# Optimization experiments

Measured on AMD Instinct MI355X. Metric: run time of the kernel, lower is better.

The kernel has to match this reference:

```python
import jax, jax.numpy as jnp
import numpy as np

B, N, DIN, DOUT = 8, 2048, 512, 256
NUM_BUCKETS = 20


def setup_inputs() -> dict:
    key = jax.random.key(0)
    ks = jax.random.split(key, 12)
    s_in = 1.0 / np.sqrt(DIN)
    s_out = 1.0 / np.sqrt(DOUT)
    return {
        "x": jax.random.normal(ks[0], (B, N, DIN), dtype=jnp.float32),
        "price_rank": jax.random.randint(ks[1], (B, N), 0, N, dtype=jnp.int64),
        "Wq": jax.random.uniform(ks[2], (DOUT, DIN), jnp.float32, -s_in, s_in),
        "bq": jax.random.uniform(ks[3], (DOUT,), jnp.float32, -s_in, s_in),
        "Wk": jax.random.uniform(ks[4], (DOUT, DIN), jnp.float32, -s_in, s_in),
        "bk": jax.random.uniform(ks[5], (DOUT,), jnp.float32, -s_in, s_in),
        "Wv": jax.random.uniform(ks[6], (DOUT, DIN), jnp.float32, -s_in, s_in),
        "bv": jax.random.uniform(ks[7], (DOUT,), jnp.float32, -s_in, s_in),
        "Ws": jax.random.uniform(ks[8], (1, DOUT), jnp.float32, -s_out, s_out),
        "bs": jax.random.uniform(ks[9], (1,), jnp.float32, -s_out, s_out),
        "rank_emb": jax.random.normal(ks[10], (NUM_BUCKETS, 1), dtype=jnp.float32),
        "rank_w": jnp.ones((1,), dtype=jnp.float32),
    }


def reference(x, price_rank, Wq, bq, Wk, bk, Wv, bv, Ws, bs, rank_emb, rank_w):
    scale = jnp.sqrt(jnp.asarray(DOUT, dtype=x.dtype))
    q = jnp.einsum("bnd,od->bno", x, Wq) + bq  # [B,N,DOUT]
    k = jnp.einsum("bnd,od->bno", x, Wk) + bk
    v = jnp.einsum("bnd,od->bno", x, Wv) + bv
    scores = jnp.einsum("bno,bmo->bnm", q, k) / scale  # [B,N,N]
    # learned pairwise rank-distance bias gate
    rank_dist = jnp.abs(price_rank[:, :, None] - price_rank[:, None, :])
    buckets = jnp.clip(rank_dist // 5, 0, NUM_BUCKETS - 1)  # [B,N,N] int
    prior = rank_emb[buckets, 0]  # gather embedding, squeeze last dim
    gate = jax.nn.sigmoid(rank_w[0] * prior)
    scores = scores * gate
    attn = jax.nn.softmax(scores, axis=2)
    context = jnp.einsum("bnm,bmo->bno", attn, v)  # [B,N,DOUT]
    winner = jax.nn.sigmoid(jnp.einsum("bno,uo->bnu", context, Ws) + bs)[..., 0]
    return winner  # [B,N]
```

## Files before the change

kernel.cpp:

```cpp
#include <hip/hip_runtime.h>
#include <hip/hip_bf16.h>

#define B_    8
#define N_    2048
#define DIN_  512
#define DOUT_ 256
#define NBUCK 20

typedef __attribute__((ext_vector_type(8))) short  short8;
typedef __attribute__((ext_vector_type(4))) float  floatx4;

__device__ __forceinline__ unsigned short f2b(float f) {
    __hip_bfloat16 h = __float2bfloat16(f);
    unsigned short u;
    __builtin_memcpy(&u, &h, 2);
    return u;
}

__device__ __forceinline__ void load_lds16(const unsigned short* g, unsigned short* l) {
    __builtin_amdgcn_global_load_lds(
        (const __attribute__((address_space(1))) unsigned int*)g,
        (__attribute__((address_space(3))) unsigned int*)l, 16, 0, 0);
}

__device__ __forceinline__ float fexp2(float x) {
    float r;
    asm("v_exp_f32 %0, %1" : "=v"(r) : "v"(x));
    return r;
}

__global__ __launch_bounds__(256) void prep_kernel(
    const float* __restrict__ Wv, const float* __restrict__ Ws,
    const float* __restrict__ bv,
    float* __restrict__ wvs, float* __restrict__ bvs) {
    const int blk = blockIdx.x, tid = threadIdx.x;
    __shared__ float wsl[DOUT_];
    wsl[tid] = Ws[tid];
    __syncthreads();
    if (tid < 128) {
        int d = blk * 128 + tid;
        float s0 = 0.f, s1 = 0.f, s2 = 0.f, s3 = 0.f;
#pragma unroll 8
        for (int o = 0; o < DOUT_; o += 4) {
            s0 += Wv[(size_t)(o + 0) * DIN_ + d] * wsl[o + 0];
            s1 += Wv[(size_t)(o + 1) * DIN_ + d] * wsl[o + 1];
            s2 += Wv[(size_t)(o + 2) * DIN_ + d] * wsl[o + 2];
            s3 += Wv[(size_t)(o + 3) * DIN_ + d] * wsl[o + 3];
        }
        wvs[d] = (s0 + s1) + (s2 + s3);
    }
    if (blk == 0 && tid < 64) {
        float bb = wsl[tid] * bv[tid] + wsl[tid + 64] * bv[tid + 64] +
                   wsl[tid + 128] * bv[tid + 128] + wsl[tid + 192] * bv[tid + 192];
        for (int off = 1; off < 64; off <<= 1) bb += __shfl_xor(bb, off, 64);
        if (tid == 0) *bvs = bb;
    }
}

__global__ __launch_bounds__(256) void cvt_x_kernel(const float* __restrict__ x,
                                                    const float* __restrict__ wvs,
                                                    const float* __restrict__ bvs,
                                                    const float* __restrict__ wq,
                                                    const float* __restrict__ wk,
                                                    unsigned short* __restrict__ xb,
                                                    unsigned short* __restrict__ wdst,
                                                    float* __restrict__ vw) {
    int tid = threadIdx.x;
    if (blockIdx.x >= 4096) {
        int i = ((blockIdx.x - 4096) * 256 + tid) * 8;
        const float* src = (i < 131072) ? (wq + i) : (wk + (i - 131072));
        float4 a = *(const float4*)(src);
        float4 b = *(const float4*)(src + 4);
        uint4 r;
        r.x = f2b(a.x) | ((unsigned)f2b(a.y) << 16);
        r.y = f2b(a.z) | ((unsigned)f2b(a.w) << 16);
        r.z = f2b(b.x) | ((unsigned)f2b(b.y) << 16);
        r.w = f2b(b.z) | ((unsigned)f2b(b.w) << 16);
        *(uint4*)(wdst + i) = r;
        return;
    }
    int wave = tid >> 6, lane = tid & 63;
    int row = blockIdx.x * 4 + wave;
    size_t base = (size_t)row * DIN_ + lane * 8;
    float4 a = *(const float4*)(x + base);
    float4 b = *(const float4*)(x + base + 4);
    float4 wa = *(const float4*)(wvs + lane * 8);
    float4 wb = *(const float4*)(wvs + lane * 8 + 4);
    uint4 r;
    r.x = f2b(a.x) | ((unsigned)f2b(a.y) << 16);
    r.y = f2b(a.z) | ((unsigned)f2b(a.w) << 16);
    r.z = f2b(b.x) | ((unsigned)f2b(b.y) << 16);
    r.w = f2b(b.z) | ((unsigned)f2b(b.w) << 16);
    *(uint4*)(xb + base) = r;
    float d = a.x * wa.x + a.y * wa.y + a.z * wa.z + a.w * wa.w +
              b.x * wb.x + b.y * wb.y + b.z * wb.z + b.w * wb.w;
    for (int off = 1; off < 64; off <<= 1) d += __shfl_xor(d, off, 64);
    if (lane == 0) vw[row] = d + *bvs;
}

__global__ __launch_bounds__(256, 2) void qkv_kernel(
    const unsigned short* __restrict__ xb, const unsigned short* __restrict__ wb,
    const float* __restrict__ bq, const float* __restrict__ bk,
    unsigned short* __restrict__ qo, unsigned short* __restrict__ ko) {
    __shared__ unsigned short alds[2][128 * 64];
    __shared__ unsigned short blds[2][128 * 64];
    const int g = blockIdx.x;
    const int xcd = g & 7, t2 = g >> 3;
    const int colBlk = t2 & 3, rowGrp = t2 >> 2;
    const int rowBlk = rowGrp * 8 + xcd;
    const int tid = threadIdx.x;
    const int wave = tid >> 6, lane = tid & 63, quad = lane >> 4, l16 = lane & 15;
    const int wr = wave >> 1, wc = wave & 1;
    const int row0 = rowBlk * 128, col0 = colBlk * 128;
    const int sw3 = l16 & 7;

    floatx4 acc[4][4];
#pragma unroll
    for (int i = 0; i < 4; ++i)
#pragma unroll
        for (int j = 0; j < 4; ++j) acc[i][j] = (floatx4){0.f, 0.f, 0.f, 0.f};

    const int gseg = (lane & 7) ^ (lane >> 3);
    const unsigned short* ag = xb + (size_t)(row0 + wave * 8 + (lane >> 3)) * DIN_ + gseg * 8;
    const unsigned short* bg = wb + (size_t)(col0 + wave * 8 + (lane >> 3)) * DIN_ + gseg * 8;

#pragma unroll
    for (int i = 0; i < 4; ++i) {
        load_lds16(ag + (size_t)i * 32 * DIN_, &alds[0][wave * 512 + i * 2048]);
        load_lds16(bg + (size_t)i * 32 * DIN_, &blds[0][wave * 512 + i * 2048]);
    }
    __syncthreads();

#pragma unroll 1
    for (int t = 0; t < 8; ++t) {
        const unsigned short* al = (t & 1) ? alds[1] : alds[0];
        const unsigned short* bl = (t & 1) ? blds[1] : blds[0];
        unsigned short* aln = (t & 1) ? &alds[0][0] : &alds[1][0];
        unsigned short* bln = (t & 1) ? &blds[0][0] : &blds[1][0];
        if (t < 7) {
            size_t koff = (size_t)(t + 1) * 64;
#pragma unroll
            for (int i = 0; i < 4; ++i) {
                load_lds16(ag + (size_t)i * 32 * DIN_ + koff, aln + wave * 512 + i * 2048);
                load_lds16(bg + (size_t)i * 32 * DIN_ + koff, bln + wave * 512 + i * 2048);
            }
        }
#pragma unroll
        for (int h = 0; h < 2; ++h) {
            short8 af[4], bf[4];
#pragma unroll
            for (int f = 0; f < 4; ++f) {
                int ar = wr * 64 + f * 16 + l16;
                int br = wc * 64 + f * 16 + l16;
                int s  = (h * 4 + quad) ^ sw3;
                af[f] = *(const short8*)&al[(size_t)ar * 64 + s * 8];
                bf[f] = *(const short8*)&bl[(size_t)br * 64 + s * 8];
            }
#pragma unroll
            for (int i = 0; i < 4; ++i)
#pragma unroll
                for (int j = 0; j < 4; ++j)
                    acc[i][j] = __builtin_amdgcn_mfma_f32_16x16x32_bf16(af[i], bf[j], acc[i][j], 0, 0, 0);
        }
        __syncthreads();
    }

#pragma unroll
    for (int j = 0; j < 4; ++j) {
        int col = col0 + wc * 64 + j * 16 + l16;
        unsigned short* dst = (col < 256) ? qo : ko;
        float bias = (col < 256) ? bq[col] : bk[col - 256];
        int c = col & 255;
#pragma unroll
        for (int i = 0; i < 4; ++i)
#pragma unroll
            for (int r = 0; r < 4; ++r) {
                int row = row0 + wr * 64 + i * 16 + quad * 4 + r;
                dst[(size_t)row * DOUT_ + c] = f2b(acc[i][j][r] + bias);
            }
    }
}

__global__ __launch_bounds__(512, 2) void attn_kernel(
    const unsigned short* __restrict__ q, const unsigned short* __restrict__ k,
    const float* __restrict__ vw, const int* __restrict__ pr,
    const float* __restrict__ rank_emb, const float* __restrict__ rank_w,
    const float* __restrict__ bs, float* __restrict__ out) {
    const int g = blockIdx.x;
    const int b = g & 7, rblk = g >> 3;
    const int tid = threadIdx.x, wave = tid >> 6, lane = tid & 63;
    const int quad = lane >> 4, l16 = lane & 15;
    const int n0 = rblk * 64;
    const int rg = wave >> 2, ch = wave & 3;

    __shared__ unsigned short kbuf[2][32768];
    __shared__ float gtab_r[NBUCK * 32];
    __shared__ float lL[8][32], wdL[8][32];

    for (int t = tid; t < NBUCK * 32; t += 512)
        gtab_r[t] = 0.0625f * 1.44269504f /
                    (1.f + __expf(-rank_w[0] * rank_emb[t >> 5]));

    const unsigned short* qb = q + (size_t)b * N_ * DOUT_;
    const unsigned short* kb = k + (size_t)b * N_ * DOUT_;
    const float* vwb = vw + b * N_;
    const int* prb = pr + b * N_;
    const int l8 = lane & 7;
    const int l31 = lane & 31;

    short8 qf[2][8];
#pragma unroll
    for (int a = 0; a < 2; ++a)
#pragma unroll
        for (int c = 0; c < 8; ++c)
            qf[a][c] = *(const short8*)(qb + (size_t)(n0 + rg * 32 + a * 16 + l16) * DOUT_ + c * 32 + quad * 8);

    float prn5[2][4];
#pragma unroll
    for (int a = 0; a < 2; ++a)
#pragma unroll
        for (int r = 0; r < 4; ++r)
            prn5[a][r] = (float)prb[n0 + rg * 32 + a * 16 + quad * 4 + r] * 0.2f;

    float lacc[2][4], wacc[2][4];
#pragma unroll
    for (int a = 0; a < 2; ++a)
#pragma unroll
        for (int r = 0; r < 4; ++r) { lacc[a][r] = 0.f; wacc[a][r] = 0.f; }

    const int stg_rbase = wave * 2 + (lane >> 5);
    const int stg_gseg  = (lane & 31) ^ (stg_rbase & 7);
    const unsigned short* stg_src0 = kb + (size_t)stg_rbase * DOUT_ + stg_gseg * 8;
    unsigned short* sdst0 = &kbuf[0][wave * 512];
    unsigned short* sdst1 = &kbuf[1][wave * 512];

    auto stage = [&](int j, unsigned short* sdst) {
        const unsigned short* src = stg_src0 + (size_t)j * 128 * DOUT_;
#pragma unroll
        for (int i = 0; i < 8; ++i)
            load_lds16(src + (size_t)i * 4096, sdst + i * 4096);
    };
    auto mfma = [&](floatx4 (&s)[2][2], const unsigned short* buf) {
#pragma unroll
        for (int a = 0; a < 2; ++a)
#pragma unroll
            for (int cf = 0; cf < 2; ++cf) s[a][cf] = (floatx4){0.f, 0.f, 0.f, 0.f};
        __builtin_amdgcn_s_setprio(1);
#pragma unroll
        for (int c = 0; c < 8; ++c) {
            int seg = (c * 4 + quad) ^ l8;
            short8 kf0 = *(const short8*)&buf[(size_t)(ch * 32 + l16) * 256 + seg * 8];
            short8 kf1 = *(const short8*)&buf[(size_t)(ch * 32 + 16 + l16) * 256 + seg * 8];
            s[0][0] = __builtin_amdgcn_mfma_f32_16x16x32_bf16(qf[0][c], kf0, s[0][0], 0, 0, 0);
            s[1][0] = __builtin_amdgcn_mfma_f32_16x16x32_bf16(qf[1][c], kf0, s[1][0], 0, 0, 0);
            s[0][1] = __builtin_amdgcn_mfma_f32_16x16x32_bf16(qf[0][c], kf1, s[0][1], 0, 0, 0);
            s[1][1] = __builtin_amdgcn_mfma_f32_16x16x32_bf16(qf[1][c], kf1, s[1][1], 0, 0, 0);
        }
        __builtin_amdgcn_s_setprio(0);
    };
    auto gate = [&](floatx4 (&s)[2][2], int pm0, int pm1, float w0, float w1) {
        float pm5_0 = (float)pm0 * 0.2f, pm5_1 = (float)pm1 * 0.2f;
#pragma unroll
        for (int a = 0; a < 2; ++a)
#pragma unroll
            for (int r = 0; r < 4; ++r) {
                float d0 = fabsf(prn5[a][r] - pm5_0);
                int i0 = (int)fminf(d0, 19.0f);
                float p0 = fexp2(s[a][0][r] * gtab_r[i0 * 32 + l31]);
                lacc[a][r] += p0;
                wacc[a][r] += p0 * w0;
                float d1 = fabsf(prn5[a][r] - pm5_1);
                int i1 = (int)fminf(d1, 19.0f);
                float p1 = fexp2(s[a][1][r] * gtab_r[i1 * 32 + l31]);
                lacc[a][r] += p1;
                wacc[a][r] += p1 * w1;
            }
    };

    floatx4 sA[2][2], sB[2][2];
    const int colq = ch * 32 + l16;

    stage(0, sdst0);
    int   pmA0 = prb[colq], pmA1 = prb[colq + 16];
    float wA0 = vwb[colq], wA1 = vwb[colq + 16];
    __syncthreads();
    stage(1, sdst1);
    int   pmB0 = prb[128 + colq], pmB1 = prb[128 + colq + 16];
    float wB0 = vwb[128 + colq], wB1 = vwb[128 + colq + 16];
    mfma(sA, kbuf[0]);
    __syncthreads();

#pragma unroll 1
    for (int jj = 0; jj < 7; ++jj) {
        {
            int jn = 2 * jj + 2;
            stage(jn, sdst0);
            int   p0 = prb[jn * 128 + colq], p1 = prb[jn * 128 + colq + 16];
            float w0 = vwb[jn * 128 + colq], w1 = vwb[jn * 128 + colq + 16];
            mfma(sB, kbuf[1]);
            __builtin_amdgcn_sched_barrier(0);
            gate(sA, pmA0, pmA1, wA0, wA1);
            pmA0 = p0; pmA1 = p1; wA0 = w0; wA1 = w1;
            __syncthreads();
        }
        {
            int jn = 2 * jj + 3;
            stage(jn, sdst1);
            int   p0 = prb[jn * 128 + colq], p1 = prb[jn * 128 + colq + 16];
            float w0 = vwb[jn * 128 + colq], w1 = vwb[jn * 128 + colq + 16];
            mfma(sA, kbuf[0]);
            __builtin_amdgcn_sched_barrier(0);
            gate(sB, pmB0, pmB1, wB0, wB1);
            pmB0 = p0; pmB1 = p1; wB0 = w0; wB1 = w1;
            __syncthreads();
        }
    }
    mfma(sB, kbuf[1]);
    __builtin_amdgcn_sched_barrier(0);
    gate(sA, pmA0, pmA1, wA0, wA1);
    gate(sB, pmB0, pmB1, wB0, wB1);

#pragma unroll
    for (int off = 1; off < 16; off <<= 1) {
#pragma unroll
        for (int a = 0; a < 2; ++a)
#pragma unroll
            for (int r = 0; r < 4; ++r) {
                lacc[a][r] += __shfl_xor(lacc[a][r], off, 64);
                wacc[a][r] += __shfl_xor(wacc[a][r], off, 64);
            }
    }
    if (l16 == 0) {
#pragma unroll
        for (int a = 0; a < 2; ++a)
#pragma unroll
            for (int r = 0; r < 4; ++r) {
                int row = a * 16 + quad * 4 + r;
                lL[wave][row]  = lacc[a][r];
                wdL[wave][row] = wacc[a][r];
            }
    }
    __syncthreads();
    if (tid < 64) {
        int rg2 = tid >> 5, sub = tid & 31;
        float l = 0.f, wd = 0.f;
#pragma unroll
        for (int c2 = 0; c2 < 4; ++c2) {
            l  += lL[rg2 * 4 + c2][sub];
            wd += wdL[rg2 * 4 + c2][sub];
        }
        float logit = wd / l + bs[0];
        out[(size_t)b * N_ + n0 + tid] = 1.f / (1.f + __expf(-logit));
    }
}

extern "C" void kernel_launch(void* const* d_in, const int* in_sizes, int n_in,
                              void* d_out, int out_size, void* d_ws, size_t ws_size,
                              hipStream_t stream) {
    const float* x   = (const float*)d_in[0];
    const int*   pr  = (const int*)d_in[1];
    const float* Wq  = (const float*)d_in[2];
    const float* bq  = (const float*)d_in[3];
    const float* Wk  = (const float*)d_in[4];
    const float* bk  = (const float*)d_in[5];
    const float* Wv  = (const float*)d_in[6];
    const float* bv  = (const float*)d_in[7];
    const float* Ws  = (const float*)d_in[8];
    const float* bs  = (const float*)d_in[9];
    const float* remb = (const float*)d_in[10];
    const float* rw   = (const float*)d_in[11];
    float* out = (float*)d_out;

    char* ws = (char*)d_ws;
    unsigned short* xb  = (unsigned short*)ws;
    unsigned short* wb  = (unsigned short*)(ws + 16777216);
    unsigned short* q   = (unsigned short*)(ws + 17301504);
    unsigned short* kk  = (unsigned short*)(ws + 25690112);
    float*          vwp = (float*)(ws + 34078720);
    float*          wvs = (float*)(ws + 34144256);
    float*          bvs = (float*)(ws + 34146304);

    hipLaunchKernelGGL(prep_kernel, dim3(4), dim3(256), 0, stream,
                       Wv, Ws, bv, wvs, bvs);
    hipLaunchKernelGGL(cvt_x_kernel, dim3(4224), dim3(256), 0, stream,
                       x, wvs, bvs, Wq, Wk, xb, wb, vwp);
    hipLaunchKernelGGL(qkv_kernel, dim3(512), dim3(256), 0, stream,
                       xb, wb, bq, bk, q, kk);
    hipLaunchKernelGGL(attn_kernel, dim3(256), dim3(512), 0, stream,
                       q, kk, vwp, pr, remb, rw, bs, out);
}
```

Measured before the change: 146.0 us.

## Fuse fp32-to-bf16 conversion and v·Ws projection into QKV GEMM kernel

Removes the separate conversion kernel and converts x and Wq/Wk from fp32 to bf16 while staging them into LDS inside the QKV GEMM. The fused v-projection dot product is accumulated by the column-block-0 workgroups. This drops the bf16 x and weight round trip through global memory and one launch. In exchange, each x row is read as fp32 by four column blocks, conversion is done in registers through a register-staged pipeline instead of direct global-to-LDS loads, and register pressure rises.

```diff
diff --git a/kernel.cpp b/kernel.cpp
--- a/kernel.cpp
+++ b/kernel.cpp
@@ -57,53 +57,15 @@
     }
 }
 
-__global__ __launch_bounds__(256) void cvt_x_kernel(const float* __restrict__ x,
-                                                    const float* __restrict__ wvs,
-                                                    const float* __restrict__ bvs,
-                                                    const float* __restrict__ wq,
-                                                    const float* __restrict__ wk,
-                                                    unsigned short* __restrict__ xb,
-                                                    unsigned short* __restrict__ wdst,
-                                                    float* __restrict__ vw) {
-    int tid = threadIdx.x;
-    if (blockIdx.x >= 4096) {
-        int i = ((blockIdx.x - 4096) * 256 + tid) * 8;
-        const float* src = (i < 131072) ? (wq + i) : (wk + (i - 131072));
-        float4 a = *(const float4*)(src);
-        float4 b = *(const float4*)(src + 4);
-        uint4 r;
-        r.x = f2b(a.x) | ((unsigned)f2b(a.y) << 16);
-        r.y = f2b(a.z) | ((unsigned)f2b(a.w) << 16);
-        r.z = f2b(b.x) | ((unsigned)f2b(b.y) << 16);
-        r.w = f2b(b.z) | ((unsigned)f2b(b.w) << 16);
-        *(uint4*)(wdst + i) = r;
-        return;
-    }
-    int wave = tid >> 6, lane = tid & 63;
-    int row = blockIdx.x * 4 + wave;
-    size_t base = (size_t)row * DIN_ + lane * 8;
-    float4 a = *(const float4*)(x + base);
-    float4 b = *(const float4*)(x + base + 4);
-    float4 wa = *(const float4*)(wvs + lane * 8);
-    float4 wb = *(const float4*)(wvs + lane * 8 + 4);
-    uint4 r;
-    r.x = f2b(a.x) | ((unsigned)f2b(a.y) << 16);
-    r.y = f2b(a.z) | ((unsigned)f2b(a.w) << 16);
-    r.z = f2b(b.x) | ((unsigned)f2b(b.y) << 16);
-    r.w = f2b(b.z) | ((unsigned)f2b(b.w) << 16);
-    *(uint4*)(xb + base) = r;
-    float d = a.x * wa.x + a.y * wa.y + a.z * wa.z + a.w * wa.w +
-              b.x * wb.x + b.y * wb.y + b.z * wb.z + b.w * wb.w;
-    for (int off = 1; off < 64; off <<= 1) d += __shfl_xor(d, off, 64);
-    if (lane == 0) vw[row] = d + *bvs;
-}
-
-__global__ __launch_bounds__(256, 2) void qkv_kernel(
-    const unsigned short* __restrict__ xb, const unsigned short* __restrict__ wb,
-    const float* __restrict__ bq, const float* __restrict__ bk,
-    unsigned short* __restrict__ qo, unsigned short* __restrict__ ko) {
-    __shared__ unsigned short alds[2][128 * 64];
-    __shared__ unsigned short blds[2][128 * 64];
+__global__ __launch_bounds__(256, 2) void qkvx_kernel(
+    const float* __restrict__ x, const float* __restrict__ wq,
+    const float* __restrict__ wk, const float* __restrict__ bq,
+    const float* __restrict__ bk, const float* __restrict__ wvs,
+    const float* __restrict__ bvs, unsigned short* __restrict__ qo,
+    unsigned short* __restrict__ ko, float* __restrict__ vw) {
+    __shared__ unsigned short alds[2][8192];
+    __shared__ unsigned short blds[2][8192];
+    __shared__ float wsl[DIN_];
     const int g = blockIdx.x;
     const int xcd = g & 7, t2 = g >> 3;
     const int colBlk = t2 & 3, rowGrp = t2 >> 2;
@@ -114,21 +76,84 @@
     const int row0 = rowBlk * 128, col0 = colBlk * 128;
     const int sw3 = l16 & 7;
 
+    wsl[tid] = wvs[tid];
+    wsl[tid + 256] = wvs[tid + 256];
+
+    const int sr = tid >> 1, h2 = tid & 1, r7 = sr & 7;
+    const float* asrc = x + (size_t)(row0 + sr) * DIN_ + h2 * 32;
+    const float* bsrc = (colBlk < 2 ? wq + (size_t)(col0 + sr) * DIN_
+                                    : wk + (size_t)(col0 + sr - 256) * DIN_) + h2 * 32;
+
     floatx4 acc[4][4];
 #pragma unroll
     for (int i = 0; i < 4; ++i)
 #pragma unroll
         for (int j = 0; j < 4; ++j) acc[i][j] = (floatx4){0.f, 0.f, 0.f, 0.f};
 
-    const int gseg = (lane & 7) ^ (lane >> 3);
-    const unsigned short* ag = xb + (size_t)(row0 + wave * 8 + (lane >> 3)) * DIN_ + gseg * 8;
-    const unsigned short* bg = wb + (size_t)(col0 + wave * 8 + (lane >> 3)) * DIN_ + gseg * 8;
-
-#pragma unroll
-    for (int i = 0; i < 4; ++i) {
-        load_lds16(ag + (size_t)i * 32 * DIN_, &alds[0][wave * 512 + i * 2048]);
-        load_lds16(bg + (size_t)i * 32 * DIN_, &blds[0][wave * 512 + i * 2048]);
-    }
+    float4 ar[8], br[8];
+    float vwacc = 0.f;
+
+    auto cvtseg = [&](const float4& a, const float4& b) -> uint4 {
+        uint4 r;
+        r.x = f2b(a.x) | ((unsigned)f2b(a.y) << 16);
+        r.y = f2b(a.z) | ((unsigned)f2b(a.w) << 16);
+        r.z = f2b(b.x) | ((unsigned)f2b(b.y) << 16);
+        r.w = f2b(b.z) | ((unsigned)f2b(b.w) << 16);
+        return r;
+    };
+    auto loadA = [&](int t) {
+        const float* s = asrc + t * 64;
+#pragma unroll
+        for (int j = 0; j < 8; ++j) ar[j] = *(const float4*)(s + j * 4);
+    };
+    auto loadB = [&](int t) {
+        const float* s = bsrc + t * 64;
+#pragma unroll
+        for (int j = 0; j < 8; ++j) br[j] = *(const float4*)(s + j * 4);
+    };
+    auto writeA = [&](unsigned short* dst) {
+#pragma unroll
+        for (int j = 0; j < 4; ++j) {
+            int p = (h2 * 4 + j) ^ r7;
+            *(uint4*)&dst[(size_t)sr * 64 + p * 8] = cvtseg(ar[2 * j], ar[2 * j + 1]);
+        }
+    };
+    auto writeB = [&](unsigned short* dst) {
+#pragma unroll
+        for (int j = 0; j < 4; ++j) {
+            int p = (h2 * 4 + j) ^ r7;
+            *(uint4*)&dst[(size_t)sr * 64 + p * 8] = cvtseg(br[2 * j], br[2 * j + 1]);
+        }
+    };
+    auto vwstep = [&](int t) {
+        if (colBlk == 0) {
+            const float* af = (const float*)ar;
+            const float* w = &wsl[t * 64 + h2 * 32];
+#pragma unroll
+            for (int m = 0; m < 32; ++m) vwacc += af[m] * w[m];
+        }
+    };
+    auto mfmah = [&](int h, const unsigned short* al, const unsigned short* bl) {
+        short8 af[4], bf[4];
+#pragma unroll
+        for (int f = 0; f < 4; ++f) {
+            int s = (h * 4 + quad) ^ sw3;
+            af[f] = *(const short8*)&al[(size_t)(wr * 64 + f * 16 + l16) * 64 + s * 8];
+            bf[f] = *(const short8*)&bl[(size_t)(wc * 64 + f * 16 + l16) * 64 + s * 8];
+        }
+#pragma unroll
+        for (int i = 0; i < 4; ++i)
+#pragma unroll
+            for (int j = 0; j < 4; ++j)
+                acc[i][j] = __builtin_amdgcn_mfma_f32_16x16x32_bf16(af[i], bf[j], acc[i][j], 0, 0, 0);
+    };
+
+    loadA(0);
+    loadB(0);
+    __syncthreads();
+    writeA(&alds[0][0]);
+    vwstep(0);
+    writeB(&blds[0][0]);
     __syncthreads();
 
 #pragma unroll 1
@@ -137,31 +162,15 @@
         const unsigned short* bl = (t & 1) ? blds[1] : blds[0];
         unsigned short* aln = (t & 1) ? &alds[0][0] : &alds[1][0];
         unsigned short* bln = (t & 1) ? &blds[0][0] : &blds[1][0];
+        if (t < 7) loadA(t + 1);
+        mfmah(0, al, bl);
         if (t < 7) {
-            size_t koff = (size_t)(t + 1) * 64;
-#pragma unroll
-            for (int i = 0; i < 4; ++i) {
-                load_lds16(ag + (size_t)i * 32 * DIN_ + koff, aln + wave * 512 + i * 2048);
-                load_lds16(bg + (size_t)i * 32 * DIN_ + koff, bln + wave * 512 + i * 2048);
-            }
-        }
-#pragma unroll
-        for (int h = 0; h < 2; ++h) {
-            short8 af[4], bf[4];
-#pragma unroll
-            for (int f = 0; f < 4; ++f) {
-                int ar = wr * 64 + f * 16 + l16;
-                int br = wc * 64 + f * 16 + l16;
-                int s  = (h * 4 + quad) ^ sw3;
-                af[f] = *(const short8*)&al[(size_t)ar * 64 + s * 8];
-                bf[f] = *(const short8*)&bl[(size_t)br * 64 + s * 8];
-            }
-#pragma unroll
-            for (int i = 0; i < 4; ++i)
-#pragma unroll
-                for (int j = 0; j < 4; ++j)
-                    acc[i][j] = __builtin_amdgcn_mfma_f32_16x16x32_bf16(af[i], bf[j], acc[i][j], 0, 0, 0);
-        }
+            writeA(aln);
+            vwstep(t + 1);
+            loadB(t + 1);
+        }
+        mfmah(1, al, bl);
+        if (t < 7) writeB(bln);
         __syncthreads();
     }
 
@@ -178,6 +187,10 @@
                 int row = row0 + wr * 64 + i * 16 + quad * 4 + r;
                 dst[(size_t)row * DOUT_ + c] = f2b(acc[i][j][r] + bias);
             }
+    }
+    if (colBlk == 0) {
+        vwacc += __shfl_xor(vwacc, 1, 64);
+        if (h2 == 0) vw[row0 + sr] = vwacc + *bvs;
     }
 }
 
@@ -372,8 +385,6 @@
     float* out = (float*)d_out;
 
     char* ws = (char*)d_ws;
-    unsigned short* xb  = (unsigned short*)ws;
-    unsigned short* wb  = (unsigned short*)(ws + 16777216);
     unsigned short* q   = (unsigned short*)(ws + 17301504);
     unsigned short* kk  = (unsigned short*)(ws + 25690112);
     float*          vwp = (float*)(ws + 34078720);
@@ -382,10 +393,8 @@
 
     hipLaunchKernelGGL(prep_kernel, dim3(4), dim3(256), 0, stream,
                        Wv, Ws, bv, wvs, bvs);
-    hipLaunchKernelGGL(cvt_x_kernel, dim3(4224), dim3(256), 0, stream,
-                       x, wvs, bvs, Wq, Wk, xb, wb, vwp);
-    hipLaunchKernelGGL(qkv_kernel, dim3(512), dim3(256), 0, stream,
-                       xb, wb, bq, bk, q, kk);
+    hipLaunchKernelGGL(qkvx_kernel, dim3(512), dim3(256), 0, stream,
+                       x, Wq, Wk, bq, bk, wvs, bvs, q, kk, vwp);
     hipLaunchKernelGGL(attn_kernel, dim3(256), dim3(512), 0, stream,
                        q, kk, vwp, pr, remb, rw, bs, out);
 }
```

New measurement: 160.2 us. +9.7%, slower.

## Fuse all four stages into one cooperative persistent kernel with grid syncs

Applied to the files above, without the earlier changes.

Replaces the four separate launches (weight prep, x/weight bf16 conversion, QKV GEMM, gated attention) with a single cooperative kernel of 256 blocks of 512 threads. Stages are separated by grid.sync(), and the GEMM runs two 256-thread tiles per block to cover the original 512 tiles. This removes launch gaps and inter-kernel drain between stages. In exchange, the grid is capped at 256 blocks with occupancy 1, so the conversion and GEMM stages lose the larger grids and two-block occupancy they had before, and grid-wide barriers add their own cost.

```diff
diff --git a/kernel.cpp b/kernel.cpp
--- a/kernel.cpp
+++ b/kernel.cpp
@@ -1,5 +1,8 @@
 #include <hip/hip_runtime.h>
+#include <hip/hip_cooperative_groups.h>
 #include <hip/hip_bf16.h>
+
+namespace cg = cooperative_groups;
 
 #define B_    8
 #define N_    2048
@@ -29,328 +32,334 @@
     return r;
 }
 
-__global__ __launch_bounds__(256) void prep_kernel(
-    const float* __restrict__ Wv, const float* __restrict__ Ws,
-    const float* __restrict__ bv,
-    float* __restrict__ wvs, float* __restrict__ bvs) {
+__global__ __launch_bounds__(512, 1) void mega_kernel(
+    const float* __restrict__ x, const int* __restrict__ pr,
+    const float* __restrict__ Wq, const float* __restrict__ bq,
+    const float* __restrict__ Wk, const float* __restrict__ bk,
+    const float* __restrict__ Wv, const float* __restrict__ bv,
+    const float* __restrict__ Ws, const float* __restrict__ bs,
+    const float* __restrict__ remb, const float* __restrict__ rw,
+    unsigned short* __restrict__ xb, unsigned short* __restrict__ wb,
+    unsigned short* __restrict__ qo, unsigned short* __restrict__ ko,
+    float* __restrict__ vwp, float* __restrict__ wvs,
+    float* __restrict__ bvs, float* __restrict__ out) {
+    __shared__ __align__(16) char smem[135680];
+    cg::grid_group grid = cg::this_grid();
     const int blk = blockIdx.x, tid = threadIdx.x;
-    __shared__ float wsl[DOUT_];
-    wsl[tid] = Ws[tid];
-    __syncthreads();
-    if (tid < 128) {
-        int d = blk * 128 + tid;
-        float s0 = 0.f, s1 = 0.f, s2 = 0.f, s3 = 0.f;
+    const int half = tid >> 8, t256 = tid & 255;
+
+    {
+        float* wsl = (float*)smem;
+        if (blk < 4 && tid < 256) wsl[tid] = Ws[tid];
+        __syncthreads();
+        if (blk < 4 && tid < 128) {
+            int d = blk * 128 + tid;
+            float s0 = 0.f, s1 = 0.f, s2 = 0.f, s3 = 0.f;
 #pragma unroll 8
-        for (int o = 0; o < DOUT_; o += 4) {
-            s0 += Wv[(size_t)(o + 0) * DIN_ + d] * wsl[o + 0];
-            s1 += Wv[(size_t)(o + 1) * DIN_ + d] * wsl[o + 1];
-            s2 += Wv[(size_t)(o + 2) * DIN_ + d] * wsl[o + 2];
-            s3 += Wv[(size_t)(o + 3) * DIN_ + d] * wsl[o + 3];
-        }
-        wvs[d] = (s0 + s1) + (s2 + s3);
+            for (int o = 0; o < DOUT_; o += 4) {
+                s0 += Wv[(size_t)(o + 0) * DIN_ + d] * wsl[o + 0];
+                s1 += Wv[(size_t)(o + 1) * DIN_ + d] * wsl[o + 1];
+                s2 += Wv[(size_t)(o + 2) * DIN_ + d] * wsl[o + 2];
+                s3 += Wv[(size_t)(o + 3) * DIN_ + d] * wsl[o + 3];
+            }
+            wvs[d] = (s0 + s1) + (s2 + s3);
+        }
+        if (blk == 0 && tid < 64) {
+            float bb = wsl[tid] * bv[tid] + wsl[tid + 64] * bv[tid + 64] +
+                       wsl[tid + 128] * bv[tid + 128] + wsl[tid + 192] * bv[tid + 192];
+            for (int off = 1; off < 64; off <<= 1) bb += __shfl_xor(bb, off, 64);
+            if (tid == 0) *bvs = bb;
+        }
     }
-    if (blk == 0 && tid < 64) {
-        float bb = wsl[tid] * bv[tid] + wsl[tid + 64] * bv[tid + 64] +
-                   wsl[tid + 128] * bv[tid + 128] + wsl[tid + 192] * bv[tid + 192];
-        for (int off = 1; off < 64; off <<= 1) bb += __shfl_xor(bb, off, 64);
-        if (tid == 0) *bvs = bb;
+    grid.sync();
+
+    {
+#pragma unroll 1
+        for (int it = 0; it < 9; ++it) {
+            int v = it * 512 + blk * 2 + half;
+            if (v >= 4224) break;
+            if (v < 4096) {
+                int wave = t256 >> 6, lane = t256 & 63;
+                int row = v * 4 + wave;
+                size_t base = (size_t)row * DIN_ + lane * 8;
+                float4 a = *(const float4*)(x + base);
+                float4 b = *(const float4*)(x + base + 4);
+                float4 wa = *(const float4*)(wvs + lane * 8);
+                float4 wb4 = *(const float4*)(wvs + lane * 8 + 4);
+                uint4 r;
+                r.x = f2b(a.x) | ((unsigned)f2b(a.y) << 16);
+                r.y = f2b(a.z) | ((unsigned)f2b(a.w) << 16);
+                r.z = f2b(b.x) | ((unsigned)f2b(b.y) << 16);
+                r.w = f2b(b.z) | ((unsigned)f2b(b.w) << 16);
+                *(uint4*)(xb + base) = r;
+                float d = a.x * wa.x + a.y * wa.y + a.z * wa.z + a.w * wa.w +
+                          b.x * wb4.x + b.y * wb4.y + b.z * wb4.z + b.w * wb4.w;
+                for (int off = 1; off < 64; off <<= 1) d += __shfl_xor(d, off, 64);
+                if (lane == 0) vwp[row] = d + *bvs;
+            } else {
+                int i = ((v - 4096) * 256 + t256) * 8;
+                const float* src = (i < 131072) ? (Wq + i) : (Wk + (i - 131072));
+                float4 a = *(const float4*)(src);
+                float4 b = *(const float4*)(src + 4);
+                uint4 r;
+                r.x = f2b(a.x) | ((unsigned)f2b(a.y) << 16);
+                r.y = f2b(a.z) | ((unsigned)f2b(a.w) << 16);
+                r.z = f2b(b.x) | ((unsigned)f2b(b.y) << 16);
+                r.w = f2b(b.z) | ((unsigned)f2b(b.w) << 16);
+                *(uint4*)(wb + i) = r;
+            }
+        }
     }
-}
-
-__global__ __launch_bounds__(256) void cvt_x_kernel(const float* __restrict__ x,
-                                                    const float* __restrict__ wvs,
-                                                    const float* __restrict__ bvs,
-                                                    const float* __restrict__ wq,
-                                                    const float* __restrict__ wk,
-                                                    unsigned short* __restrict__ xb,
-                                                    unsigned short* __restrict__ wdst,
-                                                    float* __restrict__ vw) {
-    int tid = threadIdx.x;
-    if (blockIdx.x >= 4096) {
-        int i = ((blockIdx.x - 4096) * 256 + tid) * 8;
-        const float* src = (i < 131072) ? (wq + i) : (wk + (i - 131072));
-        float4 a = *(const float4*)(src);
-        float4 b = *(const float4*)(src + 4);
-        uint4 r;
-        r.x = f2b(a.x) | ((unsigned)f2b(a.y) << 16);
-        r.y = f2b(a.z) | ((unsigned)f2b(a.w) << 16);
-        r.z = f2b(b.x) | ((unsigned)f2b(b.y) << 16);
-        r.w = f2b(b.z) | ((unsigned)f2b(b.w) << 16);
-        *(uint4*)(wdst + i) = r;
-        return;
+    grid.sync();
+
+    {
+        unsigned short* Abuf = (unsigned short*)(smem + half * 65536);
+        unsigned short* Bbuf = Abuf + 16384;
+        const int g2 = blk * 2 + half;
+        const int xcd = g2 & 7, t2 = g2 >> 3;
+        const int colBlk = t2 & 3, rowGrp = t2 >> 2;
+        const int rowBlk = rowGrp * 8 + xcd;
+        const int wave = t256 >> 6, lane = t256 & 63, quad = lane >> 4, l16 = lane & 15;
+        const int wr = wave >> 1, wc = wave & 1;
+        const int row0 = rowBlk * 128, col0 = colBlk * 128;
+        const int sw3 = l16 & 7;
+
+        floatx4 acc[4][4];
+#pragma unroll
+        for (int i = 0; i < 4; ++i)
+#pragma unroll
+            for (int j = 0; j < 4; ++j) acc[i][j] = (floatx4){0.f, 0.f, 0.f, 0.f};
+
+        const int gseg = (lane & 7) ^ (lane >> 3);
+        const unsigned short* ag = xb + (size_t)(row0 + wave * 8 + (lane >> 3)) * DIN_ + gseg * 8;
+        const unsigned short* bg = wb + (size_t)(col0 + wave * 8 + (lane >> 3)) * DIN_ + gseg * 8;
+
+#pragma unroll
+        for (int i = 0; i < 4; ++i) {
+            load_lds16(ag + (size_t)i * 32 * DIN_, &Abuf[wave * 512 + i * 2048]);
+            load_lds16(bg + (size_t)i * 32 * DIN_, &Bbuf[wave * 512 + i * 2048]);
+        }
+        __syncthreads();
+
+#pragma unroll 1
+        for (int t = 0; t < 8; ++t) {
+            const unsigned short* al = Abuf + (t & 1) * 8192;
+            const unsigned short* bl = Bbuf + (t & 1) * 8192;
+            unsigned short* aln = Abuf + ((t & 1) ^ 1) * 8192;
+            unsigned short* bln = Bbuf + ((t & 1) ^ 1) * 8192;
+            if (t < 7) {
+                size_t koff = (size_t)(t + 1) * 64;
+#pragma unroll
+                for (int i = 0; i < 4; ++i) {
+                    load_lds16(ag + (size_t)i * 32 * DIN_ + koff, aln + wave * 512 + i * 2048);
+                    load_lds16(bg + (size_t)i * 32 * DIN_ + koff, bln + wave * 512 + i * 2048);
+                }
+            }
+#pragma unroll
+            for (int h = 0; h < 2; ++h) {
+                short8 af[4], bf[4];
+#pragma unroll
+                for (int f = 0; f < 4; ++f) {
+                    int ar = wr * 64 + f * 16 + l16;
+                    int br = wc * 64 + f * 16 + l16;
+                    int s = (h * 4 + quad) ^ sw3;
+                    af[f] = *(const short8*)&al[(size_t)ar * 64 + s * 8];
+                    bf[f] = *(const short8*)&bl[(size_t)br * 64 + s * 8];
+                }
+#pragma unroll
+                for (int i = 0; i < 4; ++i)
+#pragma unroll
+                    for (int j = 0; j < 4; ++j)
+                        acc[i][j] = __builtin_amdgcn_mfma_f32_16x16x32_bf16(af[i], bf[j], acc[i][j], 0, 0, 0);
+            }
+            __syncthreads();
+        }
+
+#pragma unroll
+        for (int j = 0; j < 4; ++j) {
+            int col = col0 + wc * 64 + j * 16 + l16;
+            unsigned short* dst = (col < 256) ? qo : ko;
+            float bias = (col < 256) ? bq[col] : bk[col - 256];
+            int c = col & 255;
+#pragma unroll
+            for (int i = 0; i < 4; ++i)
+#pragma unroll
+                for (int r = 0; r < 4; ++r) {
+                    int row = row0 + wr * 64 + i * 16 + quad * 4 + r;
+                    dst[(size_t)row * DOUT_ + c] = f2b(acc[i][j][r] + bias);
+                }
+        }
     }
-    int wave = tid >> 6, lane = tid & 63;
-    int row = blockIdx.x * 4 + wave;
-    size_t base = (size_t)row * DIN_ + lane * 8;
-    float4 a = *(const float4*)(x + base);
-    float4 b = *(const float4*)(x + base + 4);
-    float4 wa = *(const float4*)(wvs + lane * 8);
-    float4 wb = *(const float4*)(wvs + lane * 8 + 4);
-    uint4 r;
-    r.x = f2b(a.x) | ((unsigned)f2b(a.y) << 16);
-    r.y = f2b(a.z) | ((unsigned)f2b(a.w) << 16);
-    r.z = f2b(b.x) | ((unsigned)f2b(b.y) << 16);
-    r.w = f2b(b.z) | ((unsigned)f2b(b.w) << 16);
-    *(uint4*)(xb + base) = r;
-    float d = a.x * wa.x + a.y * wa.y + a.z * wa.z + a.w * wa.w +
-              b.x * wb.x + b.y * wb.y + b.z * wb.z + b.w * wb.w;
-    for (int off = 1; off < 64; off <<= 1) d += __shfl_xor(d, off, 64);
-    if (lane == 0) vw[row] = d + *bvs;
-}
-
-__global__ __launch_bounds__(256, 2) void qkv_kernel(
-    const unsigned short* __restrict__ xb, const unsigned short* __restrict__ wb,
-    const float* __restrict__ bq, const float* __restrict__ bk,
-    unsigned short* __restrict__ qo, unsigned short* __restrict__ ko) {
-    __shared__ unsigned short alds[2][128 * 64];
-    __shared__ unsigned short blds[2][128 * 64];
-    const int g = blockIdx.x;
-    const int xcd = g & 7, t2 = g >> 3;
-    const int colBlk = t2 & 3, rowGrp = t2 >> 2;
-    const int rowBlk = rowGrp * 8 + xcd;
-    const int tid = threadIdx.x;
-    const int wave = tid >> 6, lane = tid & 63, quad = lane >> 4, l16 = lane & 15;
-    const int wr = wave >> 1, wc = wave & 1;
-    const int row0 = rowBlk * 128, col0 = colBlk * 128;
-    const int sw3 = l16 & 7;
-
-    floatx4 acc[4][4];
-#pragma unroll
-    for (int i = 0; i < 4; ++i)
-#pragma unroll
-        for (int j = 0; j < 4; ++j) acc[i][j] = (floatx4){0.f, 0.f, 0.f, 0.f};
-
-    const int gseg = (lane & 7) ^ (lane >> 3);
-    const unsigned short* ag = xb + (size_t)(row0 + wave * 8 + (lane >> 3)) * DIN_ + gseg * 8;
-    const unsigned short* bg = wb + (size_t)(col0 + wave * 8 + (lane >> 3)) * DIN_ + gseg * 8;
-
-#pragma unroll
-    for (int i = 0; i < 4; ++i) {
-        load_lds16(ag + (size_t)i * 32 * DIN_, &alds[0][wave * 512 + i * 2048]);
-        load_lds16(bg + (size_t)i * 32 * DIN_, &blds[0][wave * 512 + i * 2048]);
-    }
-    __syncthreads();
+    grid.sync();
+
+    {
+        unsigned short* kb0 = (unsigned short*)smem;
+        unsigned short* kb1 = kb0 + 32768;
+        float* gtab_r = (float*)(smem + 131072);
+        float(*lL)[32] = (float(*)[32])(smem + 133632);
+        float(*wdL)[32] = (float(*)[32])(smem + 134656);
+
+        const int b = blk & 7, rblk = blk >> 3;
+        const int wave = tid >> 6, lane = tid & 63;
+        const int quad = lane >> 4, l16 = lane & 15;
+        const int n0 = rblk * 64;
+        const int rg = wave >> 2, ch = wave & 3;
+
+        for (int t = tid; t < NBUCK * 32; t += 512)
+            gtab_r[t] = 0.0625f * 1.44269504f /
+                        (1.f + __expf(-rw[0] * remb[t >> 5]));
+
+        const unsigned short* qb = qo + (size_t)b * N_ * DOUT_;
+        const unsigned short* kbp = ko + (size_t)b * N_ * DOUT_;
+        const float* vwb = vwp + b * N_;
+        const int* prb = pr + b * N_;
+        const int l8 = lane & 7;
+        const int l31 = lane & 31;
+
+        short8 qf[2][8];
+#pragma unroll
+        for (int a = 0; a < 2; ++a)
+#pragma unroll
+            for (int c = 0; c < 8; ++c)
+                qf[a][c] = *(const short8*)(qb + (size_t)(n0 + rg * 32 + a * 16 + l16) * DOUT_ + c * 32 + quad * 8);
+
+        float prn5[2][4];
+#pragma unroll
+        for (int a = 0; a < 2; ++a)
+#pragma unroll
+            for (int r = 0; r < 4; ++r)
+                prn5[a][r] = (float)prb[n0 + rg * 32 + a * 16 + quad * 4 + r] * 0.2f;
+
+        float lacc[2][4], wacc[2][4];
+#pragma unroll
+        for (int a = 0; a < 2; ++a)
+#pragma unroll
+            for (int r = 0; r < 4; ++r) { lacc[a][r] = 0.f; wacc[a][r] = 0.f; }
+
+        const int stg_rbase = wave * 2 + (lane >> 5);
+        const int stg_gseg = (lane & 31) ^ (stg_rbase & 7);
+        const unsigned short* stg_src0 = kbp + (size_t)stg_rbase * DOUT_ + stg_gseg * 8;
+        unsigned short* sdst0 = kb0 + wave * 512;
+        unsigned short* sdst1 = kb1 + wave * 512;
+
+        auto stage = [&](int j, unsigned short* sdst) {
+            const unsigned short* src = stg_src0 + (size_t)j * 128 * DOUT_;
+#pragma unroll
+            for (int i = 0; i < 8; ++i)
+                load_lds16(src + (size_t)i * 4096, sdst + i * 4096);
+        };
+        auto mfma = [&](floatx4(&s)[2][2], const unsigned short* buf) {
+#pragma unroll
+            for (int a = 0; a < 2; ++a)
+#pragma unroll
+                for (int cf = 0; cf < 2; ++cf) s[a][cf] = (floatx4){0.f, 0.f, 0.f, 0.f};
+            __builtin_amdgcn_s_setprio(1);
+#pragma unroll
+            for (int c = 0; c < 8; ++c) {
+                int seg = (c * 4 + quad) ^ l8;
+                short8 kf0 = *(const short8*)&buf[(size_t)(ch * 32 + l16) * 256 + seg * 8];
+                short8 kf1 = *(const short8*)&buf[(size_t)(ch * 32 + 16 + l16) * 256 + seg * 8];
+                s[0][0] = __builtin_amdgcn_mfma_f32_16x16x32_bf16(qf[0][c], kf0, s[0][0], 0, 0, 0);
+                s[1][0] = __builtin_amdgcn_mfma_f32_16x16x32_bf16(qf[1][c], kf0, s[1][0], 0, 0, 0);
+                s[0][1] = __builtin_amdgcn_mfma_f32_16x16x32_bf16(qf[0][c], kf1, s[0][1], 0, 0, 0);
+                s[1][1] = __builtin_amdgcn_mfma_f32_16x16x32_bf16(qf[1][c], kf1, s[1][1], 0, 0, 0);
+            }
+            __builtin_amdgcn_s_setprio(0);
+        };
+        auto gate = [&](floatx4(&s)[2][2], int pm0, int pm1, float w0, float w1) {
+            float pm5_0 = (float)pm0 * 0.2f, pm5_1 = (float)pm1 * 0.2f;
+#pragma unroll
+            for (int a = 0; a < 2; ++a)
+#pragma unroll
+                for (int r = 0; r < 4; ++r) {
+                    float d0 = fabsf(prn5[a][r] - pm5_0);
+                    int i0 = (int)fminf(d0, 19.0f);
+                    float p0 = fexp2(s[a][0][r] * gtab_r[i0 * 32 + l31]);
+                    lacc[a][r] += p0;
+                    wacc[a][r] += p0 * w0;
+                    float d1 = fabsf(prn5[a][r] - pm5_1);
+                    int i1 = (int)fminf(d1, 19.0f);
+                    float p1 = fexp2(s[a][1][r] * gtab_r[i1 * 32 + l31]);
+                    lacc[a][r] += p1;
+                    wacc[a][r] += p1 * w1;
+                }
+        };
+
+        floatx4 sA[2][2], sB[2][2];
+        const int colq = ch * 32 + l16;
+
+        stage(0, sdst0);
+        int   pmA0 = prb[colq], pmA1 = prb[colq + 16];
+        float wA0 = vwb[colq], wA1 = vwb[colq + 16];
+        __syncthreads();
+        stage(1, sdst1);
+        int   pmB0 = prb[128 + colq], pmB1 = prb[128 + colq + 16];
+        float wB0 = vwb[128 + colq], wB1 = vwb[128 + colq + 16];
+        mfma(sA, kb0);
+        __syncthreads();
 
 #pragma unroll 1
-    for (int t = 0; t < 8; ++t) {
-        const unsigned short* al = (t & 1) ? alds[1] : alds[0];
-        const unsigned short* bl = (t & 1) ? blds[1] : blds[0];
-        unsigned short* aln = (t & 1) ? &alds[0][0] : &alds[1][0];
-        unsigned short* bln = (t & 1) ? &blds[0][0] : &blds[1][0];
-        if (t < 7) {
-            size_t koff = (size_t)(t + 1) * 64;
-#pragma unroll
-            for (int i = 0; i < 4; ++i) {
-                load_lds16(ag + (size_t)i * 32 * DIN_ + koff, aln + wave * 512 + i * 2048);
-                load_lds16(bg + (size_t)i * 32 * DIN_ + koff, bln + wave * 512 + i * 2048);
-            }
-        }
-#pragma unroll
-        for (int h = 0; h < 2; ++h) {
-            short8 af[4], bf[4];
-#pragma unroll
-            for (int f = 0; f < 4; ++f) {
-                int ar = wr * 64 + f * 16 + l16;
-                int br = wc * 64 + f * 16 + l16;
-                int s  = (h * 4 + quad) ^ sw3;
-                af[f] = *(const short8*)&al[(size_t)ar * 64 + s * 8];
-                bf[f] = *(const short8*)&bl[(size_t)br * 64 + s * 8];
-            }
-#pragma unroll
-            for (int i = 0; i < 4; ++i)
-#pragma unroll
-                for (int j = 0; j < 4; ++j)
-                    acc[i][j] = __builtin_amdgcn_mfma_f32_16x16x32_bf16(af[i], bf[j], acc[i][j], 0, 0, 0);
-        }
-        __syncthreads();
-    }
-
-#pragma unroll
-    for (int j = 0; j < 4; ++j) {
-        int col = col0 + wc * 64 + j * 16 + l16;
-        unsigned short* dst = (col < 256) ? qo : ko;
-        float bias = (col < 256) ? bq[col] : bk[col - 256];
-        int c = col & 255;
-#pragma unroll
-        for (int i = 0; i < 4; ++i)
-#pragma unroll
-            for (int r = 0; r < 4; ++r) {
-                int row = row0 + wr * 64 + i * 16 + quad * 4 + r;
-                dst[(size_t)row * DOUT_ + c] = f2b(acc[i][j][r] + bias);
-            }
-    }
-}
-
-__global__ __launch_bounds__(512, 2) void attn_kernel(
-    const unsigned short* __restrict__ q, const unsigned short* __restrict__ k,
-    const float* __restrict__ vw, const int* __restrict__ pr,
-    const float* __restrict__ rank_emb, const float* __restrict__ rank_w,
-    const float* __restrict__ bs, float* __restrict__ out) {
-    const int g = blockIdx.x;
-    const int b = g & 7, rblk = g >> 3;
-    const int tid = threadIdx.x, wave = tid >> 6, lane = tid & 63;
-    const int quad = lane >> 4, l16 = lane & 15;
-    const int n0 = rblk * 64;
-    const int rg = wave >> 2, ch = wave & 3;
-
-    __shared__ unsigned short kbuf[2][32768];
-    __shared__ float gtab_r[NBUCK * 32];
-    __shared__ float lL[8][32], wdL[8][32];
-
-    for (int t = tid; t < NBUCK * 32; t += 512)
-        gtab_r[t] = 0.0625f * 1.44269504f /
-                    (1.f + __expf(-rank_w[0] * rank_emb[t >> 5]));
-
-    const unsigned short* qb = q + (size_t)b * N_ * DOUT_;
-    const unsigned short* kb = k + (size_t)b * N_ * DOUT_;
-    const float* vwb = vw + b * N_;
-    const int* prb = pr + b * N_;
-    const int l8 = lane & 7;
-    const int l31 = lane & 31;
-
-    short8 qf[2][8];
-#pragma unroll
-    for (int a = 0; a < 2; ++a)
-#pragma unroll
-        for (int c = 0; c < 8; ++c)
-            qf[a][c] = *(const short8*)(qb + (size_t)(n0 + rg * 32 + a * 16 + l16) * DOUT_ + c * 32 + quad * 8);
-
-    float prn5[2][4];
-#pragma unroll
-    for (int a = 0; a < 2; ++a)
-#pragma unroll
-        for (int r = 0; r < 4; ++r)
-            prn5[a][r] = (float)prb[n0 + rg * 32 + a * 16 + quad * 4 + r] * 0.2f;
-
-    float lacc[2][4], wacc[2][4];
-#pragma unroll
-    for (int a = 0; a < 2; ++a)
-#pragma unroll
-        for (int r = 0; r < 4; ++r) { lacc[a][r] = 0.f; wacc[a][r] = 0.f; }
-
-    const int stg_rbase = wave * 2 + (lane >> 5);
-    const int stg_gseg  = (lane & 31) ^ (stg_rbase & 7);
-    const unsigned short* stg_src0 = kb + (size_t)stg_rbase * DOUT_ + stg_gseg * 8;
-    unsigned short* sdst0 = &kbuf[0][wave * 512];
-    unsigned short* sdst1 = &kbuf[1][wave * 512];
-
-    auto stage = [&](int j, unsigned short* sdst) {
-        const unsigned short* src = stg_src0 + (size_t)j * 128 * DOUT_;
-#pragma unroll
-        for (int i = 0; i < 8; ++i)
-            load_lds16(src + (size_t)i * 4096, sdst + i * 4096);
-    };
-    auto mfma = [&](floatx4 (&s)[2][2], const unsigned short* buf) {
-#pragma unroll
-        for (int a = 0; a < 2; ++a)
-#pragma unroll
-            for (int cf = 0; cf < 2; ++cf) s[a][cf] = (floatx4){0.f, 0.f, 0.f, 0.f};
-        __builtin_amdgcn_s_setprio(1);
-#pragma unroll
-        for (int c = 0; c < 8; ++c) {
-            int seg = (c * 4 + quad) ^ l8;
-            short8 kf0 = *(const short8*)&buf[(size_t)(ch * 32 + l16) * 256 + seg * 8];
-            short8 kf1 = *(const short8*)&buf[(size_t)(ch * 32 + 16 + l16) * 256 + seg * 8];
-            s[0][0] = __builtin_amdgcn_mfma_f32_16x16x32_bf16(qf[0][c], kf0, s[0][0], 0, 0, 0);
-            s[1][0] = __builtin_amdgcn_mfma_f32_16x16x32_bf16(qf[1][c], kf0, s[1][0], 0, 0, 0);
-            s[0][1] = __builtin_amdgcn_mfma_f32_16x16x32_bf16(qf[0][c], kf1, s[0][1], 0, 0, 0);
-            s[1][1] = __builtin_amdgcn_mfma_f32_16x16x32_bf16(qf[1][c], kf1, s[1][1], 0, 0, 0);
-        }
-        __builtin_amdgcn_s_setprio(0);
-    };
-    auto gate = [&](floatx4 (&s)[2][2], int pm0, int pm1, float w0, float w1) {
-        float pm5_0 = (float)pm0 * 0.2f, pm5_1 = (float)pm1 * 0.2f;
-#pragma unroll
-        for (int a = 0; a < 2; ++a)
-#pragma unroll
-            for (int r = 0; r < 4; ++r) {
-                float d0 = fabsf(prn5[a][r] - pm5_0);
-                int i0 = (int)fminf(d0, 19.0f);
-                float p0 = fexp2(s[a][0][r] * gtab_r[i0 * 32 + l31]);
-                lacc[a][r] += p0;
-                wacc[a][r] += p0 * w0;
-                float d1 = fabsf(prn5[a][r] - pm5_1);
-                int i1 = (int)fminf(d1, 19.0f);
-                float p1 = fexp2(s[a][1][r] * gtab_r[i1 * 32 + l31]);
-                lacc[a][r] += p1;
-                wacc[a][r] += p1 * w1;
-            }
-    };
-
-    floatx4 sA[2][2], sB[2][2];
-    const int colq = ch * 32 + l16;
-
-    stage(0, sdst0);
-    int   pmA0 = prb[colq], pmA1 = prb[colq + 16];
-    float wA0 = vwb[colq], wA1 = vwb[colq + 16];
-    __syncthreads();
-    stage(1, sdst1);
-    int   pmB0 = prb[128 + colq], pmB1 = prb[128 + colq + 16];
-    float wB0 = vwb[128 + colq], wB1 = vwb[128 + colq + 16];
-    mfma(sA, kbuf[0]);
-    __syncthreads();
-
-#pragma unroll 1
-    for (int jj = 0; jj < 7; ++jj) {
-        {
-            int jn = 2 * jj + 2;
-            stage(jn, sdst0);
-            int   p0 = prb[jn * 128 + colq], p1 = prb[jn * 128 + colq + 16];
-            float w0 = vwb[jn * 128 + colq], w1 = vwb[jn * 128 + colq + 16];
-            mfma(sB, kbuf[1]);
-            __builtin_amdgcn_sched_barrier(0);
-            gate(sA, pmA0, pmA1, wA0, wA1);
-            pmA0 = p0; pmA1 = p1; wA0 = w0; wA1 = w1;
-            __syncthreads();
-        }
-        {
-            int jn = 2 * jj + 3;
-            stage(jn, sdst1);
-            int   p0 = prb[jn * 128 + colq], p1 = prb[jn * 128 + colq + 16];
-            float w0 = vwb[jn * 128 + colq], w1 = vwb[jn * 128 + colq + 16];
-            mfma(sA, kbuf[0]);
-            __builtin_amdgcn_sched_barrier(0);
-            gate(sB, pmB0, pmB1, wB0, wB1);
-            pmB0 = p0; pmB1 = p1; wB0 = w0; wB1 = w1;
-            __syncthreads();
-        }
-    }
-    mfma(sB, kbuf[1]);
-    __builtin_amdgcn_sched_barrier(0);
-    gate(sA, pmA0, pmA1, wA0, wA1);
-    gate(sB, pmB0, pmB1, wB0, wB1);
-
-#pragma unroll
-    for (int off = 1; off < 16; off <<= 1) {
-#pragma unroll
-        for (int a = 0; a < 2; ++a)
-#pragma unroll
-            for (int r = 0; r < 4; ++r) {
-                lacc[a][r] += __shfl_xor(lacc[a][r], off, 64);
-                wacc[a][r] += __shfl_xor(wacc[a][r], off, 64);
-            }
-    }
-    if (l16 == 0) {
-#pragma unroll
-        for (int a = 0; a < 2; ++a)
-#pragma unroll
-            for (int r = 0; r < 4; ++r) {
-                int row = a * 16 + quad * 4 + r;
-                lL[wave][row]  = lacc[a][r];
-                wdL[wave][row] = wacc[a][r];
-            }
-    }
-    __syncthreads();
-    if (tid < 64) {
-        int rg2 = tid >> 5, sub = tid & 31;
-        float l = 0.f, wd = 0.f;
-#pragma unroll
-        for (int c2 = 0; c2 < 4; ++c2) {
-            l  += lL[rg2 * 4 + c2][sub];
-            wd += wdL[rg2 * 4 + c2][sub];
-        }
-        float logit = wd / l + bs[0];
-        out[(size_t)b * N_ + n0 + tid] = 1.f / (1.f + __expf(-logit));
+        for (int jj = 0; jj < 7; ++jj) {
+            {
+                int jn = 2 * jj + 2;
+                stage(jn, sdst0);
+                int   p0 = prb[jn * 128 + colq], p1 = prb[jn * 128 + colq + 16];
+                float w0 = vwb[jn * 128 + colq], w1 = vwb[jn * 128 + colq + 16];
+                mfma(sB, kb1);
+                __builtin_amdgcn_sched_barrier(0);
+                gate(sA, pmA0, pmA1, wA0, wA1);
+                pmA0 = p0; pmA1 = p1; wA0 = w0; wA1 = w1;
+                __syncthreads();
+            }
+            {
+                int jn = 2 * jj + 3;
+                stage(jn, sdst1);
+                int   p0 = prb[jn * 128 + colq], p1 = prb[jn * 128 + colq + 16];
+                float w0 = vwb[jn * 128 + colq], w1 = vwb[jn * 128 + colq + 16];
+                mfma(sA, kb0);
+                __builtin_amdgcn_sched_barrier(0);
+                gate(sB, pmB0, pmB1, wB0, wB1);
+                pmB0 = p0; pmB1 = p1; wB0 = w0; wB1 = w1;
+                __syncthreads();
+            }
+        }
+        mfma(sB, kb1);
+        __builtin_amdgcn_sched_barrier(0);
+        gate(sA, pmA0, pmA1, wA0, wA1);
+        gate(sB, pmB0, pmB1, wB0, wB1);
+
+#pragma unroll
+        for (int off = 1; off < 16; off <<= 1) {
+#pragma unroll
+            for (int a = 0; a < 2; ++a)
+#pragma unroll
+                for (int r = 0; r < 4; ++r) {
+                    lacc[a][r] += __shfl_xor(lacc[a][r], off, 64);
+                    wacc[a][r] += __shfl_xor(wacc[a][r], off, 64);
+                }
+        }
+        if (l16 == 0) {
+#pragma unroll
+            for (int a = 0; a < 2; ++a)
+#pragma unroll
+                for (int r = 0; r < 4; ++r) {
+                    int row = a * 16 + quad * 4 + r;
+                    lL[wave][row] = lacc[a][r];
+                    wdL[wave][row] = wacc[a][r];
+                }
+        }
+        __syncthreads();
+        if (tid < 64) {
+            int rg2 = tid >> 5, sub = tid & 31;
+            float l = 0.f, wd = 0.f;
+#pragma unroll
+            for (int c2 = 0; c2 < 4; ++c2) {
+                l += lL[rg2 * 4 + c2][sub];
+                wd += wdL[rg2 * 4 + c2][sub];
+            }
+            float logit = wd / l + bs[0];
+            out[(size_t)b * N_ + n0 + tid] = 1.f / (1.f + __expf(-logit));
+        }
     }
 }
 
@@ -380,12 +389,8 @@
     float*          wvs = (float*)(ws + 34144256);
     float*          bvs = (float*)(ws + 34146304);
 
-    hipLaunchKernelGGL(prep_kernel, dim3(4), dim3(256), 0, stream,
-                       Wv, Ws, bv, wvs, bvs);
-    hipLaunchKernelGGL(cvt_x_kernel, dim3(4224), dim3(256), 0, stream,
-                       x, wvs, bvs, Wq, Wk, xb, wb, vwp);
-    hipLaunchKernelGGL(qkv_kernel, dim3(512), dim3(256), 0, stream,
-                       xb, wb, bq, bk, q, kk);
-    hipLaunchKernelGGL(attn_kernel, dim3(256), dim3(512), 0, stream,
-                       q, kk, vwp, pr, remb, rw, bs, out);
-}
+    void* args[] = {&x, &pr, &Wq, &bq, &Wk, &bk, &Wv, &bv, &Ws, &bs,
+                    &remb, &rw, &xb, &wb, &q, &kk, &vwp, &wvs, &bvs, &out};
+    hipLaunchCooperativeKernel((void*)mega_kernel, dim3(256), dim3(512),
+                               args, 0, stream);
+}
```

After: 254.0 us. 74.0% more time.
